# Optimization experiments

Measured on AMD Instinct MI355X. Metric: run time of the kernel, lower is better.

Reference implementation:

```python
import jax, jax.numpy as jnp
import numpy as np
import math

D_MODEL = 1024
NUM_HEADS = 16
D_K = D_MODEL // NUM_HEADS
NUM_BUCKETS = 32
MAX_DISTANCE = 512  # PositionalEncoding max_len


def _relative_position_bucket(relative_position):
    # Faithful to the torch code: both signs add num_buckets//2 (==16), rp==0 adds 0.
    half = NUM_BUCKETS // 2            # 16
    max_exact = NUM_BUCKETS // 4       # 8
    base = (relative_position > 0).astype(jnp.int32) * half \
         + (relative_position < 0).astype(jnp.int32) * half
    arp = jnp.abs(relative_position)
    is_small = arp < max_exact
    safe = jnp.maximum(arp, 1).astype(jnp.float32)  # avoid log(0); masked by is_small anyway
    large = max_exact + (jnp.log(safe / max_exact)
                         / math.log(MAX_DISTANCE / max_exact)
                         * (half - max_exact)).astype(jnp.int32)  # trunc == torch .long()
    large = jnp.minimum(large, half - 1)
    return base + jnp.where(is_small, arp, large)


def compute_bias(rel_bias_table, seq_length):
    ctx = jnp.arange(seq_length, dtype=jnp.int32)[:, None]
    mem = jnp.arange(seq_length, dtype=jnp.int32)[None, :]
    buckets = _relative_position_bucket(mem - ctx)        # [S, S]
    values = rel_bias_table[buckets]                       # [S, S, H]
    return jnp.transpose(values, (2, 0, 1))[None]          # [1, H, S, S]


def setup_inputs() -> dict:
    key = jax.random.key(0)
    ks = jax.random.split(key, 12)
    B, S, D = 2, 2048, D_MODEL
    scale = 1.0 / math.sqrt(D)
    inp = {
        "query": jax.random.normal(ks[0], (B, S, D), jnp.float32),
        "key": jax.random.normal(ks[1], (B, S, D), jnp.float32),
        "value": jax.random.normal(ks[2], (B, S, D), jnp.float32),
        "Wq": jax.random.normal(ks[3], (D, D), jnp.float32) * scale,
        "bq": jnp.zeros((D,), jnp.float32),
        "Wk": jax.random.normal(ks[4], (D, D), jnp.float32) * scale,
        "bk": jnp.zeros((D,), jnp.float32),
        "Wv": jax.random.normal(ks[5], (D, D), jnp.float32) * scale,
        "bv": jnp.zeros((D,), jnp.float32),
        "Wo": jax.random.normal(ks[6], (D, D), jnp.float32) * scale,
        "bo": jnp.zeros((D,), jnp.float32),
        "rel_bias_table": jax.random.normal(ks[7], (NUM_BUCKETS, NUM_HEADS), jnp.float32) * 0.1,
    }
    return inp


def reference(query, key, value, Wq, bq, Wk, bk, Wv, bv, Wo, bo, rel_bias_table):
    B, Sq, D = query.shape
    Sk = key.shape[1]
    H, dk = NUM_HEADS, D_K
    q = (query @ Wq + bq).reshape(B, Sq, H, dk)
    k = (key @ Wk + bk).reshape(B, Sk, H, dk)
    v = (value @ Wv + bv).reshape(B, Sk, H, dk)
    scores = jnp.einsum('bqhd,bkhd->bhqk', q, k) / math.sqrt(dk)  # [B,H,Sq,Sk]
    position_bias = compute_bias(rel_bias_table, max(Sq, Sk))[:, :, :Sq, :Sk]
    scores = scores + position_bias  # broadcast over batch (torch expand)
    attn_weights = jax.nn.softmax(scores, axis=-1)
    # dropout is identity in eval / p=0
    context = jnp.einsum('bhqk,bkhd->bqhd', attn_weights, v).reshape(B, Sq, D)
    output = context @ Wo + bo
    pb = jnp.broadcast_to(position_bias, (B, H, Sq, Sk))
    return output, attn_weights, pb
```

## Files before the change

### kernel.cpp

```cpp
#include <hip/hip_runtime.h>
#include <hip/hip_bf16.h>

#define BN 2
#define SEQ 2048
#define DM 1024
#define NH 16
#define DK 64

using f32x4  = __attribute__((ext_vector_type(4))) float;
using bf16x8 = __attribute__((ext_vector_type(8))) __bf16;
using short8 = __attribute__((ext_vector_type(8))) short;

static_assert(sizeof(bf16x8) == 16, "bf16x8 must be 16B");

#define MFMA16(a, b, c) __builtin_amdgcn_mfma_f32_16x16x32_bf16(a, b, c, 0, 0, 0)

__device__ __forceinline__ unsigned short f2b(float f) {
    __hip_bfloat16 h = __float2bfloat16(f);
    return __builtin_bit_cast(unsigned short, h);
}

__device__ __forceinline__ bf16x8 load_bf8(const unsigned short* p) {
    short8 s = *reinterpret_cast<const short8*>(p);
    return __builtin_bit_cast(bf16x8, s);
}

__global__ void bias_table_kernel(const float* __restrict__ rel,
                                  float* __restrict__ bias_val) {
    int idx = blockIdx.x * 256 + threadIdx.x;
    if (idx >= NH * 4095) return;
    int h = idx / 4095;
    int dd = idx - h * 4095;
    int d = dd - 2047;
    int a = d < 0 ? -d : d;
    int bucket;
    if (a == 0) bucket = 0;
    else if (a < 8) bucket = 16 + a;
    else {
        int k = (a >= 14) + (a >= 23) + (a >= 39) + (a >= 64) +
                (a >= 108) + (a >= 182) + (a >= 305);
        bucket = 24 + k;
    }
    bias_val[h * 4095 + dd] = rel[bucket * NH + h];
}

__global__ __launch_bounds__(256) void wtrans_kernel(
        const float* __restrict__ W0, const float* __restrict__ W1,
        const float* __restrict__ W2, const float* __restrict__ W3,
        unsigned short* __restrict__ T0, unsigned short* __restrict__ T1,
        unsigned short* __restrict__ T2, unsigned short* __restrict__ T3) {
    constexpr int P = 68;
    __shared__ unsigned short lt[64 * P];
    const int mz = blockIdx.z;
    const float* W = mz == 0 ? W0 : mz == 1 ? W1 : mz == 2 ? W2 : W3;
    unsigned short* T = mz == 0 ? T0 : mz == 1 ? T1 : mz == 2 ? T2 : T3;
    const int k0 = blockIdx.x * 64, n0 = blockIdx.y * 64;
    const int tid = threadIdx.x;
#pragma unroll
    for (int p = 0; p < 4; ++p) {
        int r = p * 16 + (tid >> 4);
        int c = (tid & 15) * 4;
        float4 vv = *(const float4*)&W[(size_t)(k0 + r) * DM + n0 + c];
#pragma unroll
        for (int j = 0; j < 4; ++j) {
            int n = c + j;
            float x = j == 0 ? vv.x : j == 1 ? vv.y : j == 2 ? vv.z : vv.w;
            lt[n * P + (r ^ ((n & 7) << 3))] = f2b(x);
        }
    }
    __syncthreads();
#pragma unroll
    for (int p = 0; p < 2; ++p) {
        int rn = p * 32 + (tid >> 3);
        int ck = (tid & 7) * 8;
        int ckx = ck ^ ((rn & 7) << 3);
        ushort4 a0 = *(ushort4*)&lt[rn * P + ckx];
        ushort4 a1 = *(ushort4*)&lt[rn * P + ckx + 4];
        *(ushort4*)&T[(size_t)(n0 + rn) * DM + k0 + ck] = a0;
        *(ushort4*)&T[(size_t)(n0 + rn) * DM + k0 + ck + 4] = a1;
    }
}

__global__ __launch_bounds__(256) void qkv_gemm(
        const float* __restrict__ Aq, const float* __restrict__ Ak, const float* __restrict__ Av,
        const unsigned short* __restrict__ Wtq, const unsigned short* __restrict__ Wtk,
        const unsigned short* __restrict__ Wtv,
        const float* __restrict__ bq, const float* __restrict__ bk, const float* __restrict__ bv,
        unsigned short* __restrict__ Qp, unsigned short* __restrict__ Kh,
        unsigned short* __restrict__ Vt,
        float* __restrict__ qnorm, float* __restrict__ khpart) {
    constexpr int KP = 40;
    __shared__ unsigned short la[128 * KP];
    __shared__ unsigned short lb[128 * KP];
    const int mat = blockIdx.z;
    const float* A = mat == 0 ? Aq : mat == 1 ? Ak : Av;
    const unsigned short* Wt = mat == 0 ? Wtq : mat == 1 ? Wtk : Wtv;
    const float* bias = mat == 0 ? bq : mat == 1 ? bk : bv;
    const float outscale = mat == 0 ? 0.125f : 1.0f;
    const int tid = threadIdx.x;
    const int m0 = blockIdx.y * 128, n0 = blockIdx.x * 128;
    const int lane = tid & 63, wid = tid >> 6;
    const int wm0 = (wid >> 1) * 64, wn0 = (wid & 1) * 64;
    const int l15 = lane & 15, l4 = lane >> 4;
    f32x4 acc[4][4] = {};

    for (int kt = 0; kt < 32; ++kt) {
        const int k0 = kt * 32;
#pragma unroll
        for (int i = 0; i < 4; ++i) {
            int idx = tid + i * 256;
            int row = idx >> 3, c4 = (idx & 7) * 4;
            float4 v = *(const float4*)(A + (size_t)(m0 + row) * DM + k0 + c4);
            ushort4 u; u.x = f2b(v.x); u.y = f2b(v.y); u.z = f2b(v.z); u.w = f2b(v.w);
            *(ushort4*)&la[row * KP + c4] = u;
        }
#pragma unroll
        for (int i = 0; i < 2; ++i) {
            int idx = tid + i * 256;
            int row = idx >> 2, c8 = (idx & 3) * 8;
            *(int4*)&lb[row * KP + c8] =
                *(const int4*)&Wt[(size_t)(n0 + row) * DM + k0 + c8];
        }
        __syncthreads();
        bf16x8 af[4], bfv[4];
#pragma unroll
        for (int m = 0; m < 4; ++m)
            af[m] = load_bf8(&la[(wm0 + m * 16 + l15) * KP + l4 * 8]);
#pragma unroll
        for (int n = 0; n < 4; ++n)
            bfv[n] = load_bf8(&lb[(wn0 + n * 16 + l15) * KP + l4 * 8]);
#pragma unroll
        for (int m = 0; m < 4; ++m)
#pragma unroll
            for (int n = 0; n < 4; ++n)
                acc[m][n] = MFMA16(af[m], bfv[n], acc[m][n]);
        __syncthreads();
    }

    float bv4[4];
#pragma unroll
    for (int n = 0; n < 4; ++n) bv4[n] = bias[n0 + wn0 + n * 16 + l15];
    float nsq[4][4];
#pragma unroll
    for (int m = 0; m < 4; ++m)
#pragma unroll
        for (int r = 0; r < 4; ++r) nsq[m][r] = 0.f;

#pragma unroll
    for (int m = 0; m < 4; ++m) {
#pragma unroll
        for (int n = 0; n < 4; ++n) {
            int gcol = n0 + wn0 + n * 16 + l15;
#pragma unroll
            for (int r = 0; r < 4; ++r) {
                int grow = m0 + wm0 + m * 16 + l4 * 4 + r;
                float val = (acc[m][n][r] + bv4[n]) * outscale;
                if (mat < 2) nsq[m][r] += val * val;
                unsigned short ob = f2b(val);
                int b = grow >> 11, s = grow & 2047;
                int hh = gcol >> 6, dl = gcol & 63;
                if (mat == 0) {
                    Qp[(size_t)grow * DM + gcol] = ob;
                } else if (mat == 1) {
                    Kh[(((size_t)(b * NH + hh) * SEQ + s) << 6) + dl] = ob;
                } else {
                    Vt[(((size_t)(b * NH + hh) * DK + dl) << 11) + s] = ob;
                }
            }
        }
    }

    if (mat < 2) {
        const int hh = (n0 + wn0) >> 6;
        const int bh = ((m0 + wm0) >> 11) * NH + hh;
#pragma unroll
        for (int m = 0; m < 4; ++m)
#pragma unroll
            for (int r = 0; r < 4; ++r) {
                float s2 = nsq[m][r];
                s2 += __shfl_xor(s2, 1);
                s2 += __shfl_xor(s2, 2);
                s2 += __shfl_xor(s2, 4);
                s2 += __shfl_xor(s2, 8);
                nsq[m][r] = s2;
            }
        if (mat == 0) {
            if (l15 == 0) {
#pragma unroll
                for (int m = 0; m < 4; ++m)
#pragma unroll
                    for (int r = 0; r < 4; ++r) {
                        int grow = m0 + wm0 + m * 16 + l4 * 4 + r;
                        qnorm[bh * SEQ + (grow & 2047)] = sqrtf(nsq[m][r]);
                    }
            }
        } else {
            float rmax = 0.f;
#pragma unroll
            for (int m = 0; m < 4; ++m)
#pragma unroll
                for (int r = 0; r < 4; ++r) rmax = fmaxf(rmax, nsq[m][r]);
            rmax = fmaxf(rmax, __shfl_xor(rmax, 16));
            rmax = fmaxf(rmax, __shfl_xor(rmax, 32));
            if (lane == 0)
                khpart[bh * 32 + (((m0 + wm0) & 2047) >> 6)] = sqrtf(rmax);
        }
    }
}

__global__ __launch_bounds__(256) void o_gemm(
        const unsigned short* __restrict__ Actx, const unsigned short* __restrict__ Wto,
        const float* __restrict__ bo, float* __restrict__ out) {
    constexpr int KP = 40;
    __shared__ unsigned short la[64 * KP];
    __shared__ unsigned short lb[128 * KP];
    const int tid = threadIdx.x;
    const int m0 = blockIdx.y * 64, n0 = blockIdx.x * 128;
    const int lane = tid & 63, wid = tid >> 6;
    const int wm0 = (wid >> 1) * 32, wn0 = (wid & 1) * 64;
    const int l15 = lane & 15, l4 = lane >> 4;
    f32x4 acc[2][4] = {};

    for (int kt = 0; kt < 32; ++kt) {
        const int k0 = kt * 32;
        {
            int row = tid >> 2, c8 = (tid & 3) * 8;
            *(int4*)&la[row * KP + c8] =
                *(const int4*)&Actx[(size_t)(m0 + row) * DM + k0 + c8];
        }
#pragma unroll
        for (int i = 0; i < 2; ++i) {
            int idx = tid + i * 256;
            int row = idx >> 2, c8 = (idx & 3) * 8;
            *(int4*)&lb[row * KP + c8] =
                *(const int4*)&Wto[(size_t)(n0 + row) * DM + k0 + c8];
        }
        __syncthreads();
        bf16x8 af[2], bfv[4];
#pragma unroll
        for (int m = 0; m < 2; ++m)
            af[m] = load_bf8(&la[(wm0 + m * 16 + l15) * KP + l4 * 8]);
#pragma unroll
        for (int n = 0; n < 4; ++n)
            bfv[n] = load_bf8(&lb[(wn0 + n * 16 + l15) * KP + l4 * 8]);
#pragma unroll
        for (int m = 0; m < 2; ++m)
#pragma unroll
            for (int n = 0; n < 4; ++n)
                acc[m][n] = MFMA16(af[m], bfv[n], acc[m][n]);
        __syncthreads();
    }

#pragma unroll
    for (int m = 0; m < 2; ++m)
#pragma unroll
        for (int n = 0; n < 4; ++n) {
            int gcol = n0 + wn0 + n * 16 + l15;
            float bb = bo[gcol];
#pragma unroll
            for (int r = 0; r < 4; ++r) {
                int grow = m0 + wm0 + m * 16 + l4 * 4 + r;
                out[(size_t)grow * DM + gcol] = acc[m][n][r] + bb;
            }
        }
}

__global__ __launch_bounds__(256, 4) void attn7_kernel(
        const unsigned short* __restrict__ Qp, const unsigned short* __restrict__ Kh,
        const unsigned short* __restrict__ Vt, const float* __restrict__ bias_val,
        const float* __restrict__ qnorm, const float* __restrict__ khpart,
        float* __restrict__ attn_out, float* __restrict__ pb_out,
        unsigned short* __restrict__ ctx) {
    __shared__ float bias_lds[2112];
    __shared__ float wtile[2][4][16 * 36];
    __shared__ float redmax[4];
    const int tid = threadIdx.x;
    const int lane = tid & 63, wid = tid >> 6;
    const int l15 = lane & 15, l4 = lane >> 4;
    const int bid = (blockIdx.x & 7) * 128 + (blockIdx.x >> 3);
    const int qb = bid & 31;
    const int h = (bid >> 5) & 15;
    const int b = bid >> 9;
    const int q0 = qb * 64;
    const int qw = q0 + wid * 16;
    const int bh = b * NH + h;

    float pmax = -1e30f;
    {
        const float* bp = bias_val + h * 4095 + (2047 - (q0 + 63));
        for (int i = tid; i < 2111; i += 256) {
            float x = bp[i];
            bias_lds[i] = x;
            pmax = fmaxf(pmax, x);
        }
    }
#pragma unroll
    for (int off = 1; off < 64; off <<= 1) pmax = fmaxf(pmax, __shfl_xor(pmax, off));
    if (lane == 0) redmax[wid] = pmax;
    __syncthreads();
    const float bmax = fmaxf(fmaxf(redmax[0], redmax[1]), fmaxf(redmax[2], redmax[3]));

    float khv = (lane < 32) ? khpart[bh * 32 + lane] : 0.f;
#pragma unroll
    for (int off = 1; off < 64; off <<= 1) khv = fmaxf(khv, __shfl_xor(khv, off));

    float Mr[4];
#pragma unroll
    for (int r = 0; r < 4; ++r)
        Mr[r] = qnorm[bh * SEQ + qw + l4 * 4 + r] * 1.01f * khv + bmax + 0.1f;

    const unsigned short* qbase = Qp + (size_t)(b * SEQ + qw + l15) * DM + h * DK;
    bf16x8 qa0 = load_bf8(qbase + l4 * 8);
    bf16x8 qa1 = load_bf8(qbase + 32 + l4 * 8);

    const unsigned short* kbase = Kh + (((size_t)bh * SEQ) << 6);
    const int bbase = 63 - wid * 16 - l4 * 4;

    float lsum[4] = {0.f, 0.f, 0.f, 0.f};
    bf16x8 k00, k01, k10, k11;
    {
        const unsigned short* kp = kbase + ((size_t)l15 << 6);
        k00 = load_bf8(kp + l4 * 8);
        k01 = load_bf8(kp + 32 + l4 * 8);
        k10 = load_bf8(kp + (16 << 6) + l4 * 8);
        k11 = load_bf8(kp + (16 << 6) + 32 + l4 * 8);
    }
    for (int c0 = 0; c0 < SEQ; c0 += 32) {
        f32x4 a0 = {}, a1 = {};
        a0 = MFMA16(qa0, k00, a0); a0 = MFMA16(qa1, k01, a0);
        a1 = MFMA16(qa0, k10, a1); a1 = MFMA16(qa1, k11, a1);
        const int cn = (c0 + 32) & (SEQ - 1);
        const unsigned short* kp = kbase + ((size_t)(cn + l15) << 6);
        k00 = load_bf8(kp + l4 * 8);
        k01 = load_bf8(kp + 32 + l4 * 8);
        k10 = load_bf8(kp + (16 << 6) + l4 * 8);
        k11 = load_bf8(kp + (16 << 6) + 32 + l4 * 8);
#pragma unroll
        for (int r = 0; r < 4; ++r) {
            float e0 = __expf(a0[r] + bias_lds[c0 + l15 + bbase - r] - Mr[r]);
            float e1 = __expf(a1[r] + bias_lds[c0 + 16 + l15 + bbase - r] - Mr[r]);
            lsum[r] += e0 + e1;
        }
    }
    float Mlog[4];
#pragma unroll
    for (int r = 0; r < 4; ++r) {
        float s = lsum[r];
        s += __shfl_xor(s, 1);
        s += __shfl_xor(s, 2);
        s += __shfl_xor(s, 4);
        s += __shfl_xor(s, 8);
        Mlog[r] = Mr[r] + __logf(s);
    }

    float* abase = attn_out + ((size_t)(bh * SEQ + qw)) * SEQ;
    float* pbase = pb_out + ((size_t)(bh * SEQ + qw)) * SEQ;
    const unsigned short* vbase = Vt + (((size_t)bh * DK) << 11);
    f32x4 cacc[4] = {};

    {
        const unsigned short* kp = kbase + ((size_t)l15 << 6);
        k00 = load_bf8(kp + l4 * 8);
        k01 = load_bf8(kp + 32 + l4 * 8);
        k10 = load_bf8(kp + (16 << 6) + l4 * 8);
        k11 = load_bf8(kp + (16 << 6) + 32 + l4 * 8);
    }
    const int srow = lane >> 2, scg = (lane & 3) * 8;
    int cur = 0;
    for (int c0 = 0; c0 < SEQ; c0 += 32, cur ^= 1) {
        f32x4 a0 = {}, a1 = {};
        a0 = MFMA16(qa0, k00, a0); a0 = MFMA16(qa1, k01, a0);
        a1 = MFMA16(qa0, k10, a1); a1 = MFMA16(qa1, k11, a1);
        const int cn = (c0 + 32) & (SEQ - 1);
        const unsigned short* kp = kbase + ((size_t)(cn + l15) << 6);
        k00 = load_bf8(kp + l4 * 8);
        k01 = load_bf8(kp + 32 + l4 * 8);
        k10 = load_bf8(kp + (16 << 6) + l4 * 8);
        k11 = load_bf8(kp + (16 << 6) + 32 + l4 * 8);
        bf16x8 vv0 = load_bf8(vbase + ((size_t)(0 * 16 + l15) << 11) + c0 + l4 * 8);
        bf16x8 vv1 = load_bf8(vbase + ((size_t)(1 * 16 + l15) << 11) + c0 + l4 * 8);
        bf16x8 vv2 = load_bf8(vbase + ((size_t)(2 * 16 + l15) << 11) + c0 + l4 * 8);
        bf16x8 vv3 = load_bf8(vbase + ((size_t)(3 * 16 + l15) << 11) + c0 + l4 * 8);
        float* wt = wtile[cur][wid];
#pragma unroll
        for (int r = 0; r < 4; ++r) {
            int row = l4 * 4 + r;
            float w0 = __expf(a0[r] + bias_lds[c0 + l15 + bbase - r] - Mlog[r]);
            float w1 = __expf(a1[r] + bias_lds[c0 + 16 + l15 + bbase - r] - Mlog[r]);
            wt[row * 36 + l15] = w0;
            wt[row * 36 + 16 + l15] = w1;
        }
        asm volatile("s_waitcnt lgkmcnt(0)" ::: "memory");
        __builtin_amdgcn_sched_barrier(0);
        {
            float4 v0 = *(const float4*)&wt[srow * 36 + scg];
            float4 v1 = *(const float4*)&wt[srow * 36 + scg + 4];
            float* gp = abase + (size_t)srow * SEQ + c0 + scg;
            *(float4*)gp = v0;
            *(float4*)(gp + 4) = v1;
        }
        {
            const int ib = c0 + scg + (63 - wid * 16) - srow;
            float4 p0, p1;
            p0.x = bias_lds[ib + 0]; p0.y = bias_lds[ib + 1];
            p0.z = bias_lds[ib + 2]; p0.w = bias_lds[ib + 3];
            p1.x = bias_lds[ib + 4]; p1.y = bias_lds[ib + 5];
            p1.z = bias_lds[ib + 6]; p1.w = bias_lds[ib + 7];
            float* gp = pbase + (size_t)srow * SEQ + c0 + scg;
            *(float4*)gp = p0;
            *(float4*)(gp + 4) = p1;
        }
        float4 pA = *(const float4*)&wt[l15 * 36 + l4 * 8];
        float4 pB = *(const float4*)&wt[l15 * 36 + l4 * 8 + 4];
        short8 ps;
        ps[0] = (short)f2b(pA.x); ps[1] = (short)f2b(pA.y);
        ps[2] = (short)f2b(pA.z); ps[3] = (short)f2b(pA.w);
        ps[4] = (short)f2b(pB.x); ps[5] = (short)f2b(pB.y);
        ps[6] = (short)f2b(pB.z); ps[7] = (short)f2b(pB.w);
        bf16x8 pf = __builtin_bit_cast(bf16x8, ps);
        cacc[0] = MFMA16(pf, vv0, cacc[0]);
        cacc[1] = MFMA16(pf, vv1, cacc[1]);
        cacc[2] = MFMA16(pf, vv2, cacc[2]);
        cacc[3] = MFMA16(pf, vv3, cacc[3]);
    }
#pragma unroll
    for (int d0 = 0; d0 < 4; ++d0)
#pragma unroll
        for (int r = 0; r < 4; ++r)
            ctx[(size_t)(b * SEQ + qw + l4 * 4 + r) * DM + h * DK + d0 * 16 + l15] =
                f2b(cacc[d0][r]);
}

extern "C" void kernel_launch(void* const* d_in, const int* in_sizes, int n_in,
                              void* d_out, int out_size, void* d_ws, size_t ws_size,
                              hipStream_t stream) {
    const float* query = (const float*)d_in[0];
    const float* key   = (const float*)d_in[1];
    const float* value = (const float*)d_in[2];
    const float* Wq = (const float*)d_in[3];
    const float* bq = (const float*)d_in[4];
    const float* Wk = (const float*)d_in[5];
    const float* bk = (const float*)d_in[6];
    const float* Wv = (const float*)d_in[7];
    const float* bv = (const float*)d_in[8];
    const float* Wo = (const float*)d_in[9];
    const float* bo = (const float*)d_in[10];
    const float* rel = (const float*)d_in[11];

    float* out = (float*)d_out;
    float* attn_out = out + (size_t)BN * SEQ * DM;
    float* pb_out = attn_out + (size_t)BN * NH * SEQ * SEQ;

    char* ws = (char*)d_ws;
    float* bias_val = (float*)ws;
    unsigned short* Qp  = (unsigned short*)(ws + 262144);
    unsigned short* Kh  = Qp + (size_t)BN * SEQ * DM;
    unsigned short* Vt  = Kh + (size_t)BN * SEQ * DM;
    unsigned short* ctx = Vt + (size_t)BN * SEQ * DM;
    unsigned short* Wtq = ctx + (size_t)BN * SEQ * DM;
    unsigned short* Wtk = Wtq + (size_t)DM * DM;
    unsigned short* Wtv = Wtk + (size_t)DM * DM;
    unsigned short* Wto = Wtv + (size_t)DM * DM;
    float* qnorm = (float*)(Wto + (size_t)DM * DM);
    float* khpart = qnorm + (size_t)BN * NH * SEQ;

    bias_table_kernel<<<256, 256, 0, stream>>>(rel, bias_val);
    wtrans_kernel<<<dim3(16, 16, 4), 256, 0, stream>>>(Wq, Wk, Wv, Wo, Wtq, Wtk, Wtv, Wto);
    qkv_gemm<<<dim3(8, 32, 3), 256, 0, stream>>>(query, key, value, Wtq, Wtk, Wtv,
                                                 bq, bk, bv, Qp, Kh, Vt, qnorm, khpart);
    attn7_kernel<<<BN * NH * (SEQ / 64), 256, 0, stream>>>(Qp, Kh, Vt, bias_val,
                                                           qnorm, khpart,
                                                           attn_out, pb_out, ctx);
    o_gemm<<<dim3(8, 64), 256, 0, stream>>>(ctx, Wto, bo, out);
}
```

Before: 632.4 us.

## Fuse row-sum pass with PV accumulation, defer normalization and store attn/bias afterward

The attention kernel now computes the unnormalized exponentials against a fixed upper-bound max while accumulating both the row sums and the P·V product in a single pass, then scales the context by the inverse sum. A second pass recomputes QK and writes the normalized attention weights and position bias directly to global memory without the LDS staging tile. This aims to overlap the softmax denominator pass with the PV matmul instead of doing it as a separate sweep. The trade-off is that the global stores are now narrower per-lane 16-wide scattered writes rather than float4 rows from LDS, which may reduce store coalescing.

```diff
diff --git a/kernel.cpp b/kernel.cpp
--- a/kernel.cpp
+++ b/kernel.cpp
@@ -265,7 +265,7 @@
         }
 }
 
-__global__ __launch_bounds__(256, 4) void attn7_kernel(
+__global__ __launch_bounds__(256, 4) void attn9_kernel(
         const unsigned short* __restrict__ Qp, const unsigned short* __restrict__ Kh,
         const unsigned short* __restrict__ Vt, const float* __restrict__ bias_val,
         const float* __restrict__ qnorm, const float* __restrict__ khpart,
@@ -314,9 +314,11 @@
     bf16x8 qa1 = load_bf8(qbase + 32 + l4 * 8);
 
     const unsigned short* kbase = Kh + (((size_t)bh * SEQ) << 6);
+    const unsigned short* vbase = Vt + (((size_t)bh * DK) << 11);
     const int bbase = 63 - wid * 16 - l4 * 4;
 
     float lsum[4] = {0.f, 0.f, 0.f, 0.f};
+    f32x4 cacc[4] = {};
     bf16x8 k00, k01, k10, k11;
     {
         const unsigned short* kp = kbase + ((size_t)l15 << 6);
@@ -325,47 +327,6 @@
         k10 = load_bf8(kp + (16 << 6) + l4 * 8);
         k11 = load_bf8(kp + (16 << 6) + 32 + l4 * 8);
     }
-    for (int c0 = 0; c0 < SEQ; c0 += 32) {
-        f32x4 a0 = {}, a1 = {};
-        a0 = MFMA16(qa0, k00, a0); a0 = MFMA16(qa1, k01, a0);
-        a1 = MFMA16(qa0, k10, a1); a1 = MFMA16(qa1, k11, a1);
-        const int cn = (c0 + 32) & (SEQ - 1);
-        const unsigned short* kp = kbase + ((size_t)(cn + l15) << 6);
-        k00 = load_bf8(kp + l4 * 8);
-        k01 = load_bf8(kp + 32 + l4 * 8);
-        k10 = load_bf8(kp + (16 << 6) + l4 * 8);
-        k11 = load_bf8(kp + (16 << 6) + 32 + l4 * 8);
-#pragma unroll
-        for (int r = 0; r < 4; ++r) {
-            float e0 = __expf(a0[r] + bias_lds[c0 + l15 + bbase - r] - Mr[r]);
-            float e1 = __expf(a1[r] + bias_lds[c0 + 16 + l15 + bbase - r] - Mr[r]);
-            lsum[r] += e0 + e1;
-        }
-    }
-    float Mlog[4];
-#pragma unroll
-    for (int r = 0; r < 4; ++r) {
-        float s = lsum[r];
-        s += __shfl_xor(s, 1);
-        s += __shfl_xor(s, 2);
-        s += __shfl_xor(s, 4);
-        s += __shfl_xor(s, 8);
-        Mlog[r] = Mr[r] + __logf(s);
-    }
-
-    float* abase = attn_out + ((size_t)(bh * SEQ + qw)) * SEQ;
-    float* pbase = pb_out + ((size_t)(bh * SEQ + qw)) * SEQ;
-    const unsigned short* vbase = Vt + (((size_t)bh * DK) << 11);
-    f32x4 cacc[4] = {};
-
-    {
-        const unsigned short* kp = kbase + ((size_t)l15 << 6);
-        k00 = load_bf8(kp + l4 * 8);
-        k01 = load_bf8(kp + 32 + l4 * 8);
-        k10 = load_bf8(kp + (16 << 6) + l4 * 8);
-        k11 = load_bf8(kp + (16 << 6) + 32 + l4 * 8);
-    }
-    const int srow = lane >> 2, scg = (lane & 3) * 8;
     int cur = 0;
     for (int c0 = 0; c0 < SEQ; c0 += 32, cur ^= 1) {
         f32x4 a0 = {}, a1 = {};
@@ -385,31 +346,14 @@
 #pragma unroll
         for (int r = 0; r < 4; ++r) {
             int row = l4 * 4 + r;
-            float w0 = __expf(a0[r] + bias_lds[c0 + l15 + bbase - r] - Mlog[r]);
-            float w1 = __expf(a1[r] + bias_lds[c0 + 16 + l15 + bbase - r] - Mlog[r]);
-            wt[row * 36 + l15] = w0;
-            wt[row * 36 + 16 + l15] = w1;
+            float e0 = __expf(a0[r] + bias_lds[c0 + l15 + bbase - r] - Mr[r]);
+            float e1 = __expf(a1[r] + bias_lds[c0 + 16 + l15 + bbase - r] - Mr[r]);
+            lsum[r] += e0 + e1;
+            wt[row * 36 + l15] = e0;
+            wt[row * 36 + 16 + l15] = e1;
         }
         asm volatile("s_waitcnt lgkmcnt(0)" ::: "memory");
         __builtin_amdgcn_sched_barrier(0);
-        {
-            float4 v0 = *(const float4*)&wt[srow * 36 + scg];
-            float4 v1 = *(const float4*)&wt[srow * 36 + scg + 4];
-            float* gp = abase + (size_t)srow * SEQ + c0 + scg;
-            *(float4*)gp = v0;
-            *(float4*)(gp + 4) = v1;
-        }
-        {
-            const int ib = c0 + scg + (63 - wid * 16) - srow;
-            float4 p0, p1;
-            p0.x = bias_lds[ib + 0]; p0.y = bias_lds[ib + 1];
-            p0.z = bias_lds[ib + 2]; p0.w = bias_lds[ib + 3];
-            p1.x = bias_lds[ib + 4]; p1.y = bias_lds[ib + 5];
-            p1.z = bias_lds[ib + 6]; p1.w = bias_lds[ib + 7];
-            float* gp = pbase + (size_t)srow * SEQ + c0 + scg;
-            *(float4*)gp = p0;
-            *(float4*)(gp + 4) = p1;
-        }
         float4 pA = *(const float4*)&wt[l15 * 36 + l4 * 8];
         float4 pB = *(const float4*)&wt[l15 * 36 + l4 * 8 + 4];
         short8 ps;
@@ -423,12 +367,57 @@
         cacc[2] = MFMA16(pf, vv2, cacc[2]);
         cacc[3] = MFMA16(pf, vv3, cacc[3]);
     }
+
+    float invl[4], Mlog[4];
+#pragma unroll
+    for (int r = 0; r < 4; ++r) {
+        float s = lsum[r];
+        s += __shfl_xor(s, 1);
+        s += __shfl_xor(s, 2);
+        s += __shfl_xor(s, 4);
+        s += __shfl_xor(s, 8);
+        invl[r] = 1.0f / s;
+        Mlog[r] = Mr[r] + __logf(s);
+    }
 #pragma unroll
     for (int d0 = 0; d0 < 4; ++d0)
 #pragma unroll
         for (int r = 0; r < 4; ++r)
             ctx[(size_t)(b * SEQ + qw + l4 * 4 + r) * DM + h * DK + d0 * 16 + l15] =
-                f2b(cacc[d0][r]);
+                f2b(cacc[d0][r] * invl[r]);
+
+    float* abase = attn_out + ((size_t)(bh * SEQ + qw)) * SEQ;
+    float* pbase = pb_out + ((size_t)(bh * SEQ + qw)) * SEQ;
+    {
+        const unsigned short* kp = kbase + ((size_t)l15 << 6);
+        k00 = load_bf8(kp + l4 * 8);
+        k01 = load_bf8(kp + 32 + l4 * 8);
+        k10 = load_bf8(kp + (16 << 6) + l4 * 8);
+        k11 = load_bf8(kp + (16 << 6) + 32 + l4 * 8);
+    }
+    for (int c0 = 0; c0 < SEQ; c0 += 32) {
+        f32x4 a0 = {}, a1 = {};
+        a0 = MFMA16(qa0, k00, a0); a0 = MFMA16(qa1, k01, a0);
+        a1 = MFMA16(qa0, k10, a1); a1 = MFMA16(qa1, k11, a1);
+        const int cn = (c0 + 32) & (SEQ - 1);
+        const unsigned short* kp = kbase + ((size_t)(cn + l15) << 6);
+        k00 = load_bf8(kp + l4 * 8);
+        k01 = load_bf8(kp + 32 + l4 * 8);
+        k10 = load_bf8(kp + (16 << 6) + l4 * 8);
+        k11 = load_bf8(kp + (16 << 6) + 32 + l4 * 8);
+#pragma unroll
+        for (int r = 0; r < 4; ++r) {
+            const int row = l4 * 4 + r;
+            float b0 = bias_lds[c0 + l15 + bbase - r];
+            float b1 = bias_lds[c0 + 16 + l15 + bbase - r];
+            float w0 = __expf(a0[r] + b0 - Mlog[r]);
+            float w1 = __expf(a1[r] + b1 - Mlog[r]);
+            float* ga = abase + (size_t)row * SEQ + c0 + l15;
+            float* gp = pbase + (size_t)row * SEQ + c0 + l15;
+            ga[0] = w0; ga[16] = w1;
+            gp[0] = b0; gp[16] = b1;
+        }
+    }
 }
 
 extern "C" void kernel_launch(void* const* d_in, const int* in_sizes, int n_in,
@@ -468,7 +457,7 @@
     wtrans_kernel<<<dim3(16, 16, 4), 256, 0, stream>>>(Wq, Wk, Wv, Wo, Wtq, Wtk, Wtv, Wto);
     qkv_gemm<<<dim3(8, 32, 3), 256, 0, stream>>>(query, key, value, Wtq, Wtk, Wtv,
                                                  bq, bk, bv, Qp, Kh, Vt, qnorm, khpart);
-    attn7_kernel<<<BN * NH * (SEQ / 64), 256, 0, stream>>>(Qp, Kh, Vt, bias_val,
+    attn9_kernel<<<BN * NH * (SEQ / 64), 256, 0, stream>>>(Qp, Kh, Vt, bias_val,
                                                            qnorm, khpart,
                                                            attn_out, pb_out, ctx);
     o_gemm<<<dim3(8, 64), 256, 0, stream>>>(ctx, Wto, bo, out);
```

Measured after the change: 654.2 us. +3.4%, slower.
